# Performance work log

Hardware: AMD Instinct MI355X
Metric: run time of the kernel (lower is better)

The kernel has to match this reference:

```python
import jax, jax.numpy as jnp
import numpy as np

N_HEAD = 16
LN_EPS = 1e-5


def _layernorm(x, g, b):
    mu = jnp.mean(x, axis=-1, keepdims=True)
    var = jnp.mean(jnp.square(x - mu), axis=-1, keepdims=True)
    return (x - mu) * jax.lax.rsqrt(var + LN_EPS) * g + b


def setup_inputs() -> dict:
    key = jax.random.key(0)
    ks = jax.random.split(key, 8)
    B, T, C = 2, 2048, 1024
    Dff = 4 * C
    s = 0.02
    return {
        "x": jax.random.normal(ks[0], (B, T, C), jnp.float32),
        "wq": jax.random.normal(ks[1], (C, C), jnp.float32) * s,
        "wk": jax.random.normal(ks[2], (C, C), jnp.float32) * s,
        "wv": jax.random.normal(ks[3], (C, C), jnp.float32) * s,
        "w_proj": jax.random.normal(ks[4], (C, C), jnp.float32) * s,
        "b_proj": jnp.zeros((C,), jnp.float32),
        "w1": jax.random.normal(ks[5], (C, Dff), jnp.float32) * s,
        "b1": jnp.zeros((Dff,), jnp.float32),
        "w2": jax.random.normal(ks[6], (Dff, C), jnp.float32) * s,
        "b2": jnp.zeros((C,), jnp.float32),
        "g1": jnp.ones((C,), jnp.float32),
        "be1": jnp.zeros((C,), jnp.float32),
        "g2": jnp.ones((C,), jnp.float32),
        "be2": jnp.zeros((C,), jnp.float32),
    }


def reference(x, wq, wk, wv, w_proj, b_proj, w1, b1, w2, b2, g1, be1, g2, be2):
    B, T, C = x.shape
    H = N_HEAD
    hd = C // H
    # QKV projections (all heads folded into one matmul each), -> [B,H,T,hd]
    q = (x @ wq).reshape(B, T, H, hd).transpose(0, 2, 1, 3)
    k = (x @ wk).reshape(B, T, H, hd).transpose(0, 2, 1, 3)
    v = (x @ wv).reshape(B, T, H, hd).transpose(0, 2, 1, 3)
    # scaled causal attention; scale = head_size ** -0.5 as in torch source
    scores = jnp.einsum("bhqd,bhkd->bhqk", q, k) * (hd ** -0.5)
    causal = jnp.tril(jnp.ones((T, T), bool))
    scores = jnp.where(causal, scores, jnp.finfo(scores.dtype).min)
    wei = jax.nn.softmax(scores, axis=-1)
    attn = jnp.einsum("bhqk,bhkd->bhqd", wei, v)  # [B,H,T,hd]
    attn = attn.transpose(0, 2, 1, 3).reshape(B, T, C)
    y = attn @ w_proj + b_proj
    # post-LN residuals as in Block.forward
    x = _layernorm(x + y, g1, be1)
    y = jnp.maximum(x @ w1 + b1, 0.0) @ w2 + b2
    x = _layernorm(x + y, g2, be2)
    return x
```

## Files before the change

kernel.cpp:

```cpp
#include <hip/hip_runtime.h>
#include <hip/hip_bf16.h>


typedef __attribute__((ext_vector_type(8))) short bf16x8;
typedef __attribute__((ext_vector_type(4))) float f32x4;
typedef __attribute__((ext_vector_type(4))) short short4v;

__device__ inline short f2bf(float f) {
    __hip_bfloat16 h = __float2bfloat16(f);
    return *reinterpret_cast<short*>(&h);
}
__device__ inline float bf2f(short s) {
    union { unsigned u; float f; } c;
    c.u = ((unsigned)(unsigned short)s) << 16;
    return c.f;
}

__global__ __launch_bounds__(256) void mega_prep(const float* __restrict__ x,
                                                 short* __restrict__ x_bf,
                                                 const float* __restrict__ wq,
                                                 const float* __restrict__ wk,
                                                 const float* __restrict__ wv,
                                                 const float* __restrict__ wp,
                                                 short* __restrict__ wqT,
                                                 short* __restrict__ wkT,
                                                 short* __restrict__ wvT,
                                                 short* __restrict__ wpT,
                                                 const float* __restrict__ w1,
                                                 short* __restrict__ w1T,
                                                 const float* __restrict__ w2,
                                                 short* __restrict__ w2T,
                                                 float scaleq) {
    const int blk = blockIdx.x;
    const int tid = threadIdx.x;
    if (blk < 4096) {
        const int i = blk * 256 + tid;
        float4 v = *(const float4*)(x + (size_t)i * 4);
        short4v o = { f2bf(v.x), f2bf(v.y), f2bf(v.z), f2bf(v.w) };
        *(short4v*)(x_bf + (size_t)i * 4) = o;
        return;
    }
    __shared__ short tile[32][33];
    const int tx = tid & 31, ty = tid >> 5;
    const float* in;
    short* out;
    int R, C, bx, by;
    float scale = 1.0f;
    if (blk < 8192) {
        const int b2 = blk - 4096;
        const int z = b2 >> 10;
        const int rem = b2 & 1023;
        bx = rem & 31; by = rem >> 5;
        R = 1024; C = 1024;
        in = z == 0 ? wq : z == 1 ? wk : z == 2 ? wv : wp;
        out = z == 0 ? wqT : z == 1 ? wkT : z == 2 ? wvT : wpT;
        if (z == 0) scale = scaleq;
    } else if (blk < 12288) {
        const int rem = blk - 8192;
        bx = rem & 127; by = rem >> 7;
        R = 1024; C = 4096;
        in = w1; out = w1T;
    } else {
        const int rem = blk - 12288;
        bx = rem & 31; by = rem >> 5;
        R = 4096; C = 1024;
        in = w2; out = w2T;
    }
    const int c0 = bx * 32, r0 = by * 32;
    for (int i = ty; i < 32; i += 8)
        tile[i][tx] = f2bf(in[(size_t)(r0 + i) * C + c0 + tx] * scale);
    __syncthreads();
    for (int i = ty; i < 32; i += 8)
        out[(size_t)(c0 + i) * R + r0 + tx] = tile[tx][i];
}

template <int BN, int BIAS, int RELU, int OUTBF>
__device__ __forceinline__ void gemm_core(const short* __restrict__ A,
                                          const short* __restrict__ BT,
                                          const float* __restrict__ bias,
                                          void* __restrict__ Cout,
                                          int N, int K, int lda, int ldb,
                                          int gx, int w,
                                          short* As, short* Bs, bool addbias) {
    constexpr int NI = BN / 32;
    const int tid = threadIdx.x;
    const int wid = tid >> 6;
    const int lane = tid & 63;
    const int wr = wid >> 1, wc = wid & 1;
    const int row0 = (w % gx) * 128;
    const int col0 = (w / gx) * BN;
    const int lr = lane & 15;
    const int lk = (lane >> 4) * 8;
    const int sr = lane >> 3;
    const int scs = ((lane & 7) * 8) ^ (sr * 8);
    const int rsw = (lr & 7) * 8;

    f32x4 acc[4][NI] = {};
    for (int k = 0; k < K; k += 64) {
#pragma unroll
        for (int c = 0; c < 4; ++c) {
            const int ch = wid + c * 4;
            const short* ga = A + (size_t)(row0 + ch * 8 + sr) * lda + k + scs;
            __builtin_amdgcn_global_load_lds(
                (const __attribute__((address_space(1))) unsigned int*)ga,
                (__attribute__((address_space(3))) unsigned int*)(As + ch * 512), 16, 0, 0);
        }
#pragma unroll
        for (int c = 0; c < BN / 32; ++c) {
            const int ch = wid + c * 4;
            const short* gb = BT + (size_t)(col0 + ch * 8 + sr) * ldb + k + scs;
            __builtin_amdgcn_global_load_lds(
                (const __attribute__((address_space(1))) unsigned int*)gb,
                (__attribute__((address_space(3))) unsigned int*)(Bs + ch * 512), 16, 0, 0);
        }
        __syncthreads();
#pragma unroll
        for (int kk = 0; kk < 64; kk += 32) {
            const int cof = (kk + lk) ^ rsw;
            bf16x8 a[4], b[NI];
#pragma unroll
            for (int m = 0; m < 4; ++m)
                a[m] = *(const bf16x8*)(As + (wr * 64 + m * 16 + lr) * 64 + cof);
#pragma unroll
            for (int n = 0; n < NI; ++n)
                b[n] = *(const bf16x8*)(Bs + (wc * (BN / 2) + n * 16 + lr) * 64 + cof);
#pragma unroll
            for (int m = 0; m < 4; ++m)
#pragma unroll
                for (int n = 0; n < NI; ++n)
                    acc[m][n] = __builtin_amdgcn_mfma_f32_16x16x32_bf16(a[m], b[n], acc[m][n], 0, 0, 0);
        }
        __syncthreads();
    }
#pragma unroll
    for (int m = 0; m < 4; ++m) {
        int row = row0 + wr * 64 + m * 16 + (lane >> 4) * 4;
#pragma unroll
        for (int n = 0; n < NI; ++n) {
            int col = col0 + wc * (BN / 2) + n * 16 + lr;
            float bv = (BIAS && addbias) ? bias[col] : 0.0f;
#pragma unroll
            for (int r = 0; r < 4; ++r) {
                float v = acc[m][n][r] + bv;
                if (RELU) v = fmaxf(v, 0.0f);
                if (OUTBF)
                    ((short*)Cout)[(size_t)(row + r) * N + col] = f2bf(v);
                else
                    ((float*)Cout)[(size_t)(row + r) * N + col] = v;
            }
        }
    }
}

template <int BN, int BIAS, int RELU, int OUTBF>
__global__ __launch_bounds__(256) void gemm_bt(const short* __restrict__ A,
                                               const short* __restrict__ BT,
                                               const float* __restrict__ bias,
                                               void* __restrict__ Cout,
                                               int N, int K, int lda, int ldb,
                                               void* __restrict__ Cout2) {
    __shared__ short As[128 * 64];
    __shared__ short Bs[BN * 64];
    const int kz = blockIdx.z;
    if (kz) { A += K; BT += K; Cout = Cout2; }
    const int gx = gridDim.x;
    int flat = blockIdx.x + gx * blockIdx.y;
    const int nwg = gx * gridDim.y;
    int w = flat;
    if ((nwg & 7) == 0) {
        const int q = nwg >> 3;
        w = (flat & 7) * q + (flat >> 3);
    }
    gemm_core<BN, BIAS, RELU, OUTBF>(A, BT, bias, Cout, N, K, lda, ldb, gx, w, As, Bs, kz == 0);
}

#define STAGE256(KT, ASB, BSB)                                                              \
    do {                                                                                    \
        const int kof_ = (KT) * 64;                                                         \
        _Pragma("unroll") for (int l = 0; l < 4; ++l) {                                     \
            const int ch = wid * 4 + l;                                                     \
            const short* ga = A + (size_t)(row0 + ch * 8 + sr) * lda + kof_ + scs;          \
            __builtin_amdgcn_global_load_lds(                                               \
                (const __attribute__((address_space(1))) unsigned int*)ga,                  \
                (__attribute__((address_space(3))) unsigned int*)((ASB) + ch * 512), 16, 0, 0); \
            const short* gb = BT + (size_t)(col0 + ch * 8 + sr) * ldb + kof_ + scs;         \
            __builtin_amdgcn_global_load_lds(                                               \
                (const __attribute__((address_space(1))) unsigned int*)gb,                  \
                (__attribute__((address_space(3))) unsigned int*)((BSB) + ch * 512), 16, 0, 0); \
        }                                                                                   \
    } while (0)

template <int BIAS, int RELU>
__device__ __forceinline__ void gemm256_core(const short* __restrict__ A,
                                             const short* __restrict__ BT,
                                             const float* __restrict__ bias,
                                             short* __restrict__ C,
                                             int N, int K, int lda, int ldb,
                                             int row0, int col0, bool addbias,
                                             short* As0, short* As1,
                                             short* Bs0, short* Bs1) {
    const int tid = threadIdx.x;
    const int wid = tid >> 6;
    const int lane = tid & 63;
    const int wm = wid >> 2;
    const int wn = wid & 3;
    const int lr = lane & 15;
    const int lk = (lane >> 4) * 8;
    const int sr = lane >> 3;
    const int scs = ((lane & 7) * 8) ^ (sr * 8);
    const int rsw = (lr & 7) * 8;

    f32x4 acc[8][4] = {};
    STAGE256(0, As0, Bs0);
    STAGE256(1, As1, Bs1);

    const int NK = K >> 6;
#pragma unroll 1
    for (int t = 0; t < NK; ++t) {
        short* Asc = (t & 1) ? As1 : As0;
        short* Bsc = (t & 1) ? Bs1 : Bs0;
        if (t == NK - 1)
            asm volatile("s_waitcnt vmcnt(0)" ::: "memory");
        else
            asm volatile("s_waitcnt vmcnt(8)" ::: "memory");
        __builtin_amdgcn_s_barrier();
        bf16x8 bfr[4][2];
#pragma unroll
        for (int fj = 0; fj < 4; ++fj)
#pragma unroll
            for (int ks = 0; ks < 2; ++ks)
                bfr[fj][ks] = *(const bf16x8*)(&Bsc[(wn * 64 + fj * 16 + lr) * 64 +
                                                    ((ks * 32 + lk) ^ rsw)]);
#pragma unroll
        for (int p = 0; p < 4; ++p) {
            bf16x8 afr[2][2];
#pragma unroll
            for (int f = 0; f < 2; ++f)
#pragma unroll
                for (int ks = 0; ks < 2; ++ks)
                    afr[f][ks] = *(const bf16x8*)(&Asc[(wm * 128 + (p * 2 + f) * 16 + lr) * 64 +
                                                       ((ks * 32 + lk) ^ rsw)]);
            asm volatile("s_waitcnt lgkmcnt(0)" ::: "memory");
            __builtin_amdgcn_sched_barrier(0);
            if (p == 3) {
                __builtin_amdgcn_s_barrier();
                if (t + 2 < NK) STAGE256(t + 2, Asc, Bsc);
            }
            __builtin_amdgcn_s_setprio(1);
#pragma unroll
            for (int f = 0; f < 2; ++f)
#pragma unroll
                for (int fj = 0; fj < 4; ++fj)
#pragma unroll
                    for (int ks = 0; ks < 2; ++ks)
                        acc[p * 2 + f][fj] = __builtin_amdgcn_mfma_f32_16x16x32_bf16(
                            afr[f][ks], bfr[fj][ks], acc[p * 2 + f][fj], 0, 0, 0);
            __builtin_amdgcn_s_setprio(0);
            __builtin_amdgcn_s_barrier();
        }
    }
#pragma unroll
    for (int fi = 0; fi < 8; ++fi) {
        const int row = row0 + wm * 128 + fi * 16 + (lane >> 4) * 4;
#pragma unroll
        for (int fj = 0; fj < 4; ++fj) {
            const int col = col0 + wn * 64 + fj * 16 + lr;
            const float bv = (BIAS && addbias) ? bias[col] : 0.0f;
#pragma unroll
            for (int r = 0; r < 4; ++r) {
                float v = acc[fi][fj][r] + bv;
                if (RELU) v = fmaxf(v, 0.0f);
                C[(size_t)(row + r) * N + col] = f2bf(v);
            }
        }
    }
}

__global__ __launch_bounds__(512, 2) void gemm_mlp1(const short* __restrict__ A,
                                                    const short* __restrict__ BT,
                                                    const float* __restrict__ bias,
                                                    short* __restrict__ C) {
    __shared__ short As[2][256 * 64];
    __shared__ short Bs[2][256 * 64];
    const int flat = blockIdx.x;
    const int w = (flat & 7) * 32 + (flat >> 3);
    const int row0 = (w & 15) * 256;
    const int col0 = (w >> 4) * 256;
    gemm256_core<1, 1>(A, BT, bias, C, 4096, 1024, 1024, 1024, row0, col0, true,
                       As[0], As[1], Bs[0], Bs[1]);
}

__global__ __launch_bounds__(512, 2) void gemm_qkvvt(const short* __restrict__ x_bf,
                                                     const short* __restrict__ wqkT,
                                                     const short* __restrict__ wvT,
                                                     short* __restrict__ qk,
                                                     short* __restrict__ Vt) {
    __shared__ short As[2][256 * 64];
    __shared__ short Bs[2][256 * 64];
    int flat = blockIdx.x;
    if (flat < 128) {
        const int w = (flat & 7) * 16 + (flat >> 3);
        const int row0 = (w & 15) * 256;
        const int col0 = (w >> 4) * 256;
        gemm256_core<0, 0>(x_bf, wqkT, nullptr, qk, 2048, 1024, 1024, 1024,
                           row0, col0, false, As[0], As[1], Bs[0], Bs[1]);
    } else {
        flat -= 128;
        const int w = (flat & 7) * 8 + (flat >> 3);
        const int row0 = (w & 3) * 256;
        const int col0 = (w >> 2) * 256;
        gemm256_core<0, 0>(wvT, x_bf, nullptr, Vt, 4096, 1024, 1024, 1024,
                           row0, col0, false, As[0], As[1], Bs[0], Bs[1]);
    }
}

__global__ __launch_bounds__(512, 2) void gemm_mlp2(const short* __restrict__ A,
                                                    const short* __restrict__ BT,
                                                    const float* __restrict__ bias,
                                                    short* __restrict__ C0,
                                                    short* __restrict__ C1,
                                                    short* __restrict__ C2,
                                                    short* __restrict__ C3) {
    __shared__ short As[2][256 * 64];
    __shared__ short Bs[2][256 * 64];
    const int kz = blockIdx.z;
    short* C = kz == 0 ? C0 : kz == 1 ? C1 : kz == 2 ? C2 : C3;
    const int flat = blockIdx.x;
    const int w = (flat & 7) * 8 + (flat >> 3);
    const int row0 = (w & 15) * 256;
    const int col0 = (w >> 4) * 256;
    gemm256_core<1, 0>(A + kz * 1024, BT + kz * 1024, bias, C, 1024, 1024,
                       4096, 4096, row0, col0, kz == 0, As[0], As[1], Bs[0], Bs[1]);
}

#define ATT_T 2048
#define ATT_QKS 2048
#define ATT_BT 4096

#define LOADK(KF, KB)                                                                     \
    do {                                                                                  \
        const int k0_ = (KB) * 64;                                                        \
        _Pragma("unroll") for (int t = 0; t < 4; ++t) {                                   \
            const size_t krow_ = (size_t)(b * ATT_T + k0_ + 16 * t + lr) * ATT_QKS + h * 64; \
            KF[t][0] = *(const bf16x8*)(Km + krow_ + g * 8);                              \
            KF[t][1] = *(const bf16x8*)(Km + krow_ + 32 + g * 8);                         \
        }                                                                                 \
    } while (0)

#define LOADV(VF, KB)                                                                     \
    do {                                                                                  \
        const int k0_ = (KB) * 64;                                                        \
        _Pragma("unroll") for (int n = 0; n < 4; ++n)                                     \
            _Pragma("unroll") for (int ks = 0; ks < 2; ++ks)                              \
                VF[n][ks] = *(const bf16x8*)(Vt + (size_t)(h * 64 + n * 16 + lr) * ATT_BT + \
                                             b * ATT_T + k0_ + ks * 32 + g * 8);          \
    } while (0)

#define COMPUTE(KF, VF, KB)                                                               \
    do {                                                                                  \
        const int k0_ = (KB) * 64;                                                        \
        const bool edge_ = (KB) == nfull;                                                 \
        _Pragma("unroll") for (int qs = 0; qs < 2; ++qs) {                                \
            f32x4 st[4];                                                                  \
            __builtin_amdgcn_s_setprio(1);                                                \
            _Pragma("unroll") for (int t = 0; t < 4; ++t) {                               \
                f32x4 s = {};                                                             \
                s = __builtin_amdgcn_mfma_f32_16x16x32_bf16(KF[t][0], aq[qs][0], s, 0, 0, 0); \
                s = __builtin_amdgcn_mfma_f32_16x16x32_bf16(KF[t][1], aq[qs][1], s, 0, 0, 0); \
                st[t] = s;                                                                \
            }                                                                             \
            __builtin_amdgcn_s_setprio(0);                                                \
            float rst[4];                                                                 \
            _Pragma("unroll") for (int t = 0; t < 4; ++t) {                               \
                short4v pw;                                                               \
                float pr[4];                                                              \
                _Pragma("unroll") for (int r = 0; r < 4; ++r) {                           \
                    float val = st[t][r];                                                 \
                    if (edge_ && (k0_ + 16 * t + g * 4 + r > qrow[qs])) val = -3e38f;     \
                    float p = exp2f(val);                                                 \
                    pr[r] = p;                                                            \
                    pw[r] = f2bf(p);                                                      \
                }                                                                         \
                rst[t] = (pr[0] + pr[1]) + (pr[2] + pr[3]);                               \
                *(short4v*)(&Plds[wid][qs][lr][16 * t + g * 4]) = pw;                     \
            }                                                                             \
            float rs = (rst[0] + rst[1]) + (rst[2] + rst[3]);                             \
            rs += __shfl_xor(rs, 16);                                                     \
            rs += __shfl_xor(rs, 32);                                                     \
            lrun[qs] += rs;                                                               \
        }                                                                                 \
        asm volatile("s_waitcnt lgkmcnt(0)" ::: "memory");                                \
        __builtin_amdgcn_sched_barrier(0);                                                \
        __builtin_amdgcn_s_setprio(1);                                                    \
        _Pragma("unroll") for (int qs = 0; qs < 2; ++qs)                                  \
            _Pragma("unroll") for (int ks = 0; ks < 2; ++ks) {                            \
                bf16x8 pf = *(const bf16x8*)(&Plds[wid][qs][lr][ks * 32 + g * 8]);        \
                _Pragma("unroll") for (int n = 0; n < 4; ++n)                             \
                    O[qs][n] = __builtin_amdgcn_mfma_f32_16x16x32_bf16(VF[n][ks], pf, O[qs][n], 0, 0, 0); \
            }                                                                             \
        __builtin_amdgcn_s_setprio(0);                                                    \
    } while (0)

__global__ __launch_bounds__(128) void flash_attn(const short* __restrict__ Q,
                                                  const short* __restrict__ Km,
                                                  const short* __restrict__ Vt,
                                                  short* __restrict__ Oout) {
    const int f = blockIdx.x;
    const int wid = threadIdx.x >> 6;
    const int lane = threadIdx.x & 63;
    const int lr = lane & 15;
    const int g = lane >> 4;
    const int xcd = f & 7;
    const int k = f >> 3;
    const int bh = xcd * 4 + (k & 3);
    const int b = bh >> 4;
    const int h = bh & 15;
    const int pair = (k >> 2) * 2 + wid;

    __shared__ __align__(16) short Plds[2][2][16][72];

#pragma unroll 1
    for (int job = 0; job < 2; ++job) {
        const int s = job ? (63 - pair) : pair;
        const int q0 = s << 5;
        const int qrow[2] = { q0 + lr, q0 + 16 + lr };
        const int nfull = s >> 1;

        bf16x8 aq[2][2];
#pragma unroll
        for (int qs = 0; qs < 2; ++qs)
#pragma unroll
            for (int ds = 0; ds < 2; ++ds)
                aq[qs][ds] = *(const bf16x8*)(Q + (size_t)(b * ATT_T + q0 + qs * 16 + lr) * ATT_QKS +
                                              h * 64 + ds * 32 + g * 8);

        f32x4 O[2][4] = {};
        float lrun[2] = { 0.0f, 0.0f };

        bf16x8 kfA[4][2], kfB[4][2], vf[4][2];
        LOADK(kfA, 0);
        int kb = 0;
        while (true) {
            LOADV(vf, kb);
            if (kb < nfull) LOADK(kfB, kb + 1);
            COMPUTE(kfA, vf, kb);
            ++kb;
            if (kb > nfull) break;
            LOADV(vf, kb);
            if (kb < nfull) LOADK(kfA, kb + 1);
            COMPUTE(kfB, vf, kb);
            ++kb;
            if (kb > nfull) break;
        }

#pragma unroll
        for (int qs = 0; qs < 2; ++qs) {
            const float inv = 1.0f / lrun[qs];
#pragma unroll
            for (int n = 0; n < 4; ++n) {
                short4v ov;
#pragma unroll
                for (int r = 0; r < 4; ++r) ov[r] = f2bf(O[qs][n][r] * inv);
                *(short4v*)(Oout + (size_t)(b * ATT_T + q0 + qs * 16 + lr) * 1024 +
                            h * 64 + n * 16 + g * 4) = ov;
            }
        }
    }
}

template <int XB>
__global__ __launch_bounds__(256) void resid_ln(const float* __restrict__ xf,
                                                const short* __restrict__ xb,
                                                const short* __restrict__ y,
                                                const short* __restrict__ yb,
                                                const short* __restrict__ yc,
                                                const short* __restrict__ yd,
                                                const float* __restrict__ g,
                                                const float* __restrict__ be,
                                                float* __restrict__ of,
                                                short* __restrict__ ob) {
    const int row = blockIdx.x;
    const int tid = threadIdx.x;
    const size_t base = (size_t)row * 1024 + tid * 4;
    float x0, x1, x2, x3;
    if (XB) {
        short4v xv = *(const short4v*)(xb + base);
        x0 = bf2f(xv[0]); x1 = bf2f(xv[1]); x2 = bf2f(xv[2]); x3 = bf2f(xv[3]);
    } else {
        float4 xv = *(const float4*)(xf + base);
        x0 = xv.x; x1 = xv.y; x2 = xv.z; x3 = xv.w;
    }
    short4v yv = *(const short4v*)(y + base);
    float h0 = x0 + bf2f(yv[0]), h1 = x1 + bf2f(yv[1]);
    float h2 = x2 + bf2f(yv[2]), h3 = x3 + bf2f(yv[3]);
    if (yb) {
        short4v v2 = *(const short4v*)(yb + base);
        h0 += bf2f(v2[0]); h1 += bf2f(v2[1]); h2 += bf2f(v2[2]); h3 += bf2f(v2[3]);
    }
    if (yc) {
        short4v v3 = *(const short4v*)(yc + base);
        h0 += bf2f(v3[0]); h1 += bf2f(v3[1]); h2 += bf2f(v3[2]); h3 += bf2f(v3[3]);
    }
    if (yd) {
        short4v v4 = *(const short4v*)(yd + base);
        h0 += bf2f(v4[0]); h1 += bf2f(v4[1]); h2 += bf2f(v4[2]); h3 += bf2f(v4[3]);
    }
    float s = h0 + h1 + h2 + h3;
    float ss = h0 * h0 + h1 * h1 + h2 * h2 + h3 * h3;
#pragma unroll
    for (int d = 1; d < 64; d <<= 1) {
        s += __shfl_xor(s, d);
        ss += __shfl_xor(ss, d);
    }
    __shared__ float as_[4], ass_[4];
    if ((tid & 63) == 0) { as_[tid >> 6] = s; ass_[tid >> 6] = ss; }
    __syncthreads();
    s = as_[0] + as_[1] + as_[2] + as_[3];
    ss = ass_[0] + ass_[1] + ass_[2] + ass_[3];
    const float mu = s * (1.0f / 1024.0f);
    const float var = ss * (1.0f / 1024.0f) - mu * mu;
    const float rstd = rsqrtf(var + 1e-5f);
    float4 gv = *(const float4*)(g + tid * 4);
    float4 bv = *(const float4*)(be + tid * 4);
    float o0 = (h0 - mu) * rstd * gv.x + bv.x;
    float o1 = (h1 - mu) * rstd * gv.y + bv.y;
    float o2 = (h2 - mu) * rstd * gv.z + bv.z;
    float o3 = (h3 - mu) * rstd * gv.w + bv.w;
    if (of) {
        float4 ov = { o0, o1, o2, o3 };
        *(float4*)(of + base) = ov;
    }
    if (ob) {
        short4v obv = { f2bf(o0), f2bf(o1), f2bf(o2), f2bf(o3) };
        *(short4v*)(ob + base) = obv;
    }
}


extern "C" void kernel_launch(void* const* d_in, const int* in_sizes, int n_in,
                              void* d_out, int out_size, void* d_ws, size_t ws_size,
                              hipStream_t stream) {
    const float* x = (const float*)d_in[0];
    const float* wq = (const float*)d_in[1];
    const float* wk = (const float*)d_in[2];
    const float* wv = (const float*)d_in[3];
    const float* wp = (const float*)d_in[4];
    const float* bproj = (const float*)d_in[5];
    const float* w1 = (const float*)d_in[6];
    const float* b1 = (const float*)d_in[7];
    const float* w2 = (const float*)d_in[8];
    const float* b2 = (const float*)d_in[9];
    const float* g1 = (const float*)d_in[10];
    const float* be1 = (const float*)d_in[11];
    const float* g2 = (const float*)d_in[12];
    const float* be2 = (const float*)d_in[13];

    char* ws = (char*)d_ws;
    const size_t MB = 1024 * 1024;
    short* x_bf = (short*)(ws + 0);
    short* wqkT = (short*)(ws + 8 * MB);
    short* wqT = wqkT;
    short* wkT = (short*)(ws + 10 * MB);
    short* wvT = (short*)(ws + 12 * MB);
    short* w1T = (short*)(ws + 16 * MB);
    short* w2T = (short*)(ws + 24 * MB);
    short* qk  = (short*)(ws + 32 * MB);
    short* wpT = (short*)(ws + 48 * MB);
    short* Vt  = (short*)(ws + 56 * MB);
    short* hbf = (short*)(ws + 32 * MB);
    short* attn = (short*)(ws + 64 * MB);
    short* x1bf = (short*)(ws + 64 * MB);
    short* y1a = (short*)(ws + 72 * MB);
    short* y1b = (short*)(ws + 0);
    short* y2a = (short*)(ws + 72 * MB);
    short* y2b = (short*)(ws + 0);
    short* y2c = (short*)(ws + 8 * MB);
    short* y2d = (short*)(ws + 16 * MB);

    dim3 blk(256);
    const float SC = 0.125f * 1.44269504089f;

    mega_prep<<<dim3(16384), blk, 0, stream>>>(x, x_bf, wq, wk, wv, wp,
                                               wqT, wkT, wvT, wpT,
                                               w1, w1T, w2, w2T, SC);
    gemm_qkvvt<<<dim3(192), dim3(512), 0, stream>>>(x_bf, wqkT, wvT, qk, Vt);
    flash_attn<<<dim3(512), dim3(128), 0, stream>>>(qk, qk + 1024, Vt, attn);
    gemm_bt<64, 1, 0, 1><<<dim3(32, 16, 2), blk, 0, stream>>>(attn, wpT, bproj, y1a,
                                                              1024, 512, 1024, 1024, y1b);
    resid_ln<0><<<dim3(4096), blk, 0, stream>>>(x, nullptr, y1a, y1b, nullptr, nullptr,
                                                g1, be1, nullptr, x1bf);
    gemm_mlp1<<<dim3(256), dim3(512), 0, stream>>>(x1bf, w1T, b1, hbf);
    gemm_mlp2<<<dim3(64, 1, 4), dim3(512), 0, stream>>>(hbf, w2T, b2, y2a, y2b, y2c, y2d);
    resid_ln<1><<<dim3(4096), blk, 0, stream>>>(nullptr, x1bf, y2a, y2b, y2c, y2d,
                                                g2, be2, (float*)d_out, nullptr);
}
```

Measured before the change: 253.4 us.

## Split flash-attn jobs across more blocks and reuse 256-tile split-K GEMM for projection

Flash attention now launches 1024 blocks. Each wave handles one balanced query-tile pair member instead of looping over two jobs, which raises parallelism and occupancy. The output projection drops the old 128x64 tiled split-K-by-2 GEMM and uses the generalized 256x256 double-buffered split-K-by-4 kernel (gemm_z4) that is shared with MLP2. The residual LayerNorm sums four partials. This adds partial-buffer traffic and a larger workspace footprint.

```diff
diff --git a/kernel.cpp b/kernel.cpp
--- a/kernel.cpp
+++ b/kernel.cpp
@@ -74,106 +74,6 @@
         out[(size_t)(c0 + i) * R + r0 + tx] = tile[tx][i];
 }
 
-template <int BN, int BIAS, int RELU, int OUTBF>
-__device__ __forceinline__ void gemm_core(const short* __restrict__ A,
-                                          const short* __restrict__ BT,
-                                          const float* __restrict__ bias,
-                                          void* __restrict__ Cout,
-                                          int N, int K, int lda, int ldb,
-                                          int gx, int w,
-                                          short* As, short* Bs, bool addbias) {
-    constexpr int NI = BN / 32;
-    const int tid = threadIdx.x;
-    const int wid = tid >> 6;
-    const int lane = tid & 63;
-    const int wr = wid >> 1, wc = wid & 1;
-    const int row0 = (w % gx) * 128;
-    const int col0 = (w / gx) * BN;
-    const int lr = lane & 15;
-    const int lk = (lane >> 4) * 8;
-    const int sr = lane >> 3;
-    const int scs = ((lane & 7) * 8) ^ (sr * 8);
-    const int rsw = (lr & 7) * 8;
-
-    f32x4 acc[4][NI] = {};
-    for (int k = 0; k < K; k += 64) {
-#pragma unroll
-        for (int c = 0; c < 4; ++c) {
-            const int ch = wid + c * 4;
-            const short* ga = A + (size_t)(row0 + ch * 8 + sr) * lda + k + scs;
-            __builtin_amdgcn_global_load_lds(
-                (const __attribute__((address_space(1))) unsigned int*)ga,
-                (__attribute__((address_space(3))) unsigned int*)(As + ch * 512), 16, 0, 0);
-        }
-#pragma unroll
-        for (int c = 0; c < BN / 32; ++c) {
-            const int ch = wid + c * 4;
-            const short* gb = BT + (size_t)(col0 + ch * 8 + sr) * ldb + k + scs;
-            __builtin_amdgcn_global_load_lds(
-                (const __attribute__((address_space(1))) unsigned int*)gb,
-                (__attribute__((address_space(3))) unsigned int*)(Bs + ch * 512), 16, 0, 0);
-        }
-        __syncthreads();
-#pragma unroll
-        for (int kk = 0; kk < 64; kk += 32) {
-            const int cof = (kk + lk) ^ rsw;
-            bf16x8 a[4], b[NI];
-#pragma unroll
-            for (int m = 0; m < 4; ++m)
-                a[m] = *(const bf16x8*)(As + (wr * 64 + m * 16 + lr) * 64 + cof);
-#pragma unroll
-            for (int n = 0; n < NI; ++n)
-                b[n] = *(const bf16x8*)(Bs + (wc * (BN / 2) + n * 16 + lr) * 64 + cof);
-#pragma unroll
-            for (int m = 0; m < 4; ++m)
-#pragma unroll
-                for (int n = 0; n < NI; ++n)
-                    acc[m][n] = __builtin_amdgcn_mfma_f32_16x16x32_bf16(a[m], b[n], acc[m][n], 0, 0, 0);
-        }
-        __syncthreads();
-    }
-#pragma unroll
-    for (int m = 0; m < 4; ++m) {
-        int row = row0 + wr * 64 + m * 16 + (lane >> 4) * 4;
-#pragma unroll
-        for (int n = 0; n < NI; ++n) {
-            int col = col0 + wc * (BN / 2) + n * 16 + lr;
-            float bv = (BIAS && addbias) ? bias[col] : 0.0f;
-#pragma unroll
-            for (int r = 0; r < 4; ++r) {
-                float v = acc[m][n][r] + bv;
-                if (RELU) v = fmaxf(v, 0.0f);
-                if (OUTBF)
-                    ((short*)Cout)[(size_t)(row + r) * N + col] = f2bf(v);
-                else
-                    ((float*)Cout)[(size_t)(row + r) * N + col] = v;
-            }
-        }
-    }
-}
-
-template <int BN, int BIAS, int RELU, int OUTBF>
-__global__ __launch_bounds__(256) void gemm_bt(const short* __restrict__ A,
-                                               const short* __restrict__ BT,
-                                               const float* __restrict__ bias,
-                                               void* __restrict__ Cout,
-                                               int N, int K, int lda, int ldb,
-                                               void* __restrict__ Cout2) {
-    __shared__ short As[128 * 64];
-    __shared__ short Bs[BN * 64];
-    const int kz = blockIdx.z;
-    if (kz) { A += K; BT += K; Cout = Cout2; }
-    const int gx = gridDim.x;
-    int flat = blockIdx.x + gx * blockIdx.y;
-    const int nwg = gx * gridDim.y;
-    int w = flat;
-    if ((nwg & 7) == 0) {
-        const int q = nwg >> 3;
-        w = (flat & 7) * q + (flat >> 3);
-    }
-    gemm_core<BN, BIAS, RELU, OUTBF>(A, BT, bias, Cout, N, K, lda, ldb, gx, w, As, Bs, kz == 0);
-}
-
 #define STAGE256(KT, ASB, BSB)                                                              \
     do {                                                                                    \
         const int kof_ = (KT) * 64;                                                         \
@@ -314,13 +214,14 @@
     }
 }
 
-__global__ __launch_bounds__(512, 2) void gemm_mlp2(const short* __restrict__ A,
-                                                    const short* __restrict__ BT,
-                                                    const float* __restrict__ bias,
-                                                    short* __restrict__ C0,
-                                                    short* __restrict__ C1,
-                                                    short* __restrict__ C2,
-                                                    short* __restrict__ C3) {
+__global__ __launch_bounds__(512, 2) void gemm_z4(const short* __restrict__ A,
+                                                  const short* __restrict__ BT,
+                                                  const float* __restrict__ bias,
+                                                  short* __restrict__ C0,
+                                                  short* __restrict__ C1,
+                                                  short* __restrict__ C2,
+                                                  short* __restrict__ C3,
+                                                  int Kz, int lda, int ldb) {
     __shared__ short As[2][256 * 64];
     __shared__ short Bs[2][256 * 64];
     const int kz = blockIdx.z;
@@ -329,8 +230,8 @@
     const int w = (flat & 7) * 8 + (flat >> 3);
     const int row0 = (w & 15) * 256;
     const int col0 = (w >> 4) * 256;
-    gemm256_core<1, 0>(A + kz * 1024, BT + kz * 1024, bias, C, 1024, 1024,
-                       4096, 4096, row0, col0, kz == 0, As[0], As[1], Bs[0], Bs[1]);
+    gemm256_core<1, 0>(A + kz * Kz, BT + kz * Kz, bias, C, 1024, Kz,
+                       lda, ldb, row0, col0, kz == 0, As[0], As[1], Bs[0], Bs[1]);
 }
 
 #define ATT_T 2048
@@ -411,59 +312,56 @@
     const int lr = lane & 15;
     const int g = lane >> 4;
     const int xcd = f & 7;
-    const int k = f >> 3;
-    const int bh = xcd * 4 + (k & 3);
+    const int idx = f >> 3;
+    const int bh = xcd * 4 + (idx & 3);
     const int b = bh >> 4;
     const int h = bh & 15;
-    const int pair = (k >> 2) * 2 + wid;
+    const int p = idx >> 2;
+    const int s = wid ? (63 - p) : p;
 
     __shared__ __align__(16) short Plds[2][2][16][72];
 
-#pragma unroll 1
-    for (int job = 0; job < 2; ++job) {
-        const int s = job ? (63 - pair) : pair;
-        const int q0 = s << 5;
-        const int qrow[2] = { q0 + lr, q0 + 16 + lr };
-        const int nfull = s >> 1;
-
-        bf16x8 aq[2][2];
-#pragma unroll
-        for (int qs = 0; qs < 2; ++qs)
-#pragma unroll
-            for (int ds = 0; ds < 2; ++ds)
-                aq[qs][ds] = *(const bf16x8*)(Q + (size_t)(b * ATT_T + q0 + qs * 16 + lr) * ATT_QKS +
-                                              h * 64 + ds * 32 + g * 8);
-
-        f32x4 O[2][4] = {};
-        float lrun[2] = { 0.0f, 0.0f };
-
-        bf16x8 kfA[4][2], kfB[4][2], vf[4][2];
-        LOADK(kfA, 0);
-        int kb = 0;
-        while (true) {
-            LOADV(vf, kb);
-            if (kb < nfull) LOADK(kfB, kb + 1);
-            COMPUTE(kfA, vf, kb);
-            ++kb;
-            if (kb > nfull) break;
-            LOADV(vf, kb);
-            if (kb < nfull) LOADK(kfA, kb + 1);
-            COMPUTE(kfB, vf, kb);
-            ++kb;
-            if (kb > nfull) break;
-        }
-
-#pragma unroll
-        for (int qs = 0; qs < 2; ++qs) {
-            const float inv = 1.0f / lrun[qs];
-#pragma unroll
-            for (int n = 0; n < 4; ++n) {
-                short4v ov;
-#pragma unroll
-                for (int r = 0; r < 4; ++r) ov[r] = f2bf(O[qs][n][r] * inv);
-                *(short4v*)(Oout + (size_t)(b * ATT_T + q0 + qs * 16 + lr) * 1024 +
-                            h * 64 + n * 16 + g * 4) = ov;
-            }
+    const int q0 = s << 5;
+    const int qrow[2] = { q0 + lr, q0 + 16 + lr };
+    const int nfull = s >> 1;
+
+    bf16x8 aq[2][2];
+#pragma unroll
+    for (int qs = 0; qs < 2; ++qs)
+#pragma unroll
+        for (int ds = 0; ds < 2; ++ds)
+            aq[qs][ds] = *(const bf16x8*)(Q + (size_t)(b * ATT_T + q0 + qs * 16 + lr) * ATT_QKS +
+                                          h * 64 + ds * 32 + g * 8);
+
+    f32x4 O[2][4] = {};
+    float lrun[2] = { 0.0f, 0.0f };
+
+    bf16x8 kfA[4][2], kfB[4][2], vf[4][2];
+    LOADK(kfA, 0);
+    int kb = 0;
+    while (true) {
+        LOADV(vf, kb);
+        if (kb < nfull) LOADK(kfB, kb + 1);
+        COMPUTE(kfA, vf, kb);
+        ++kb;
+        if (kb > nfull) break;
+        LOADV(vf, kb);
+        if (kb < nfull) LOADK(kfA, kb + 1);
+        COMPUTE(kfB, vf, kb);
+        ++kb;
+        if (kb > nfull) break;
+    }
+
+#pragma unroll
+    for (int qs = 0; qs < 2; ++qs) {
+        const float inv = 1.0f / lrun[qs];
+#pragma unroll
+        for (int n = 0; n < 4; ++n) {
+            short4v ov;
+#pragma unroll
+            for (int r = 0; r < 4; ++r) ov[r] = f2bf(O[qs][n][r] * inv);
+            *(short4v*)(Oout + (size_t)(b * ATT_T + q0 + qs * 16 + lr) * 1024 +
+                        h * 64 + n * 16 + g * 4) = ov;
         }
     }
 }
@@ -572,6 +470,8 @@
     short* x1bf = (short*)(ws + 64 * MB);
     short* y1a = (short*)(ws + 72 * MB);
     short* y1b = (short*)(ws + 0);
+    short* y1c = (short*)(ws + 8 * MB);
+    short* y1d = (short*)(ws + 88 * MB);
     short* y2a = (short*)(ws + 72 * MB);
     short* y2b = (short*)(ws + 0);
     short* y2c = (short*)(ws + 8 * MB);
@@ -584,13 +484,14 @@
                                                wqT, wkT, wvT, wpT,
                                                w1, w1T, w2, w2T, SC);
     gemm_qkvvt<<<dim3(192), dim3(512), 0, stream>>>(x_bf, wqkT, wvT, qk, Vt);
-    flash_attn<<<dim3(512), dim3(128), 0, stream>>>(qk, qk + 1024, Vt, attn);
-    gemm_bt<64, 1, 0, 1><<<dim3(32, 16, 2), blk, 0, stream>>>(attn, wpT, bproj, y1a,
-                                                              1024, 512, 1024, 1024, y1b);
-    resid_ln<0><<<dim3(4096), blk, 0, stream>>>(x, nullptr, y1a, y1b, nullptr, nullptr,
+    flash_attn<<<dim3(1024), dim3(128), 0, stream>>>(qk, qk + 1024, Vt, attn);
+    gemm_z4<<<dim3(64, 1, 4), dim3(512), 0, stream>>>(attn, wpT, bproj,
+                                                      y1a, y1b, y1c, y1d, 256, 1024, 1024);
+    resid_ln<0><<<dim3(4096), blk, 0, stream>>>(x, nullptr, y1a, y1b, y1c, y1d,
                                                 g1, be1, nullptr, x1bf);
     gemm_mlp1<<<dim3(256), dim3(512), 0, stream>>>(x1bf, w1T, b1, hbf);
-    gemm_mlp2<<<dim3(64, 1, 4), dim3(512), 0, stream>>>(hbf, w2T, b2, y2a, y2b, y2c, y2d);
+    gemm_z4<<<dim3(64, 1, 4), dim3(512), 0, stream>>>(hbf, w2T, b2,
+                                                      y2a, y2b, y2c, y2d, 1024, 4096, 4096);
     resid_ln<1><<<dim3(4096), blk, 0, stream>>>(nullptr, x1bf, y2a, y2b, y2c, y2d,
                                                 g2, be2, (float*)d_out, nullptr);
 }
```

Result: slower. 267.0 us (+5.3%).
